# Performance work log

Measured on AMD Instinct MI355X. Metric: run time of the kernel, lower is better.

The kernel has to match this reference:

```python
import jax, jax.numpy as jnp
import numpy as np

NQ, N, C = 8192, 32768, 128


def setup_inputs() -> dict:
    key = jax.random.key(0)
    k1, k2, k3 = jax.random.split(key, 3)
    return {
        "query_pos": jax.random.normal(k1, (NQ, 3), dtype=jnp.float32),
        "neural_feat": jax.random.normal(k2, (N, C), dtype=jnp.float32),
        "neural_pos": jax.random.normal(k3, (N, 3), dtype=jnp.float32),
        "knn": 64,
    }


def _cdist(a, b):
    # Euclidean pairwise distances via the (|a|^2 + |b|^2 - 2ab) expansion.
    a2 = jnp.sum(a * a, axis=-1, keepdims=True)          # [N',1]
    b2 = jnp.sum(b * b, axis=-1)                          # [N]
    d2 = a2 + b2[None, :] - 2.0 * (a @ b.T)               # [N',N]
    return jnp.sqrt(jnp.maximum(d2, 1e-12))


def reference(query_pos, neural_feat, neural_pos, knn):
    dists = _cdist(query_pos, neural_pos)                 # [N',N]
    # torch.topk(largest=False, sorted=True) == top_k of negated dists.
    neg_vals, closest_ind = jax.lax.top_k(-dists, knn)    # [N',k]
    closest_dists = -neg_vals                             # ascending
    closest_feat = neural_feat[closest_ind]               # [N',k,C] gather
    inv_dist = 1.0 / (closest_dists + 1e-5)               # [N',k]
    retrieved_feat = jnp.sum(closest_feat * inv_dist[..., None], axis=1)  # [N',C]
    return retrieved_feat
```

## Files before the change

kernel.cpp:

```cpp
#include <hip/hip_runtime.h>
#include <math.h>

#define NQ    8192
#define NPTS  32768
#define KNN   64
#define CAP   256
#define PG    64
#define PNC   (PG*PG*PG)
#define PCELL 0.15f
#define PGINV (PG / 9.6f)
#define QG    32
#define QNC   (QG*QG*QG)
#define QGINV (QG / 9.6f)
#define GLO   (-4.8f)
#define NBLK  2048
#define TGT   (110.0f / 32768.0f)
#define PCHUNKS (PNC / 1024)
#define QCHUNKS (QNC / 1024)

__device__ __forceinline__ unsigned key_of(float f) {
  unsigned u = __float_as_uint(f);
  return (u & 0x80000000u) ? ~u : (u | 0x80000000u);
}
__device__ __forceinline__ float val_of(unsigned k) {
  unsigned u = (k & 0x80000000u) ? (k & 0x7fffffffu) : ~k;
  return __uint_as_float(u);
}
__device__ __forceinline__ int mbcnt64(unsigned long long m) {
  return __builtin_amdgcn_mbcnt_hi((unsigned)(m >> 32),
         __builtin_amdgcn_mbcnt_lo((unsigned)m, 0));
}
__device__ __forceinline__ float rflf(float x) {
  return __int_as_float(__builtin_amdgcn_readfirstlane(__float_as_int(x)));
}
__device__ __forceinline__ int rfli(int x) { return __builtin_amdgcn_readfirstlane(x); }

__device__ __forceinline__ float norm_cdf(float x) { return 0.5f * erfcf(-x * 0.70710678f); }
__device__ __forceinline__ float ball_mass(float mu, float r) {
  float a = r - mu, b = r + mu;
  float e = __expf(-0.5f * b * b) - __expf(-0.5f * a * a);
  return e / (mu * 2.50662827f) + norm_cdf(a) - norm_cdf(-mu) + norm_cdf(b) - norm_cdf(mu);
}

__device__ __forceinline__ int cidxP(float v) {
  int i = (int)floorf((v - GLO) * PGINV);
  return min(max(i, 0), PG - 1);
}
__device__ __forceinline__ int cidxQ(float v) {
  int i = (int)floorf((v - GLO) * QGINV);
  return min(max(i, 0), QG - 1);
}


__global__ __launch_bounds__(256) void hist_tau_kernel(
    const float* __restrict__ pos, const float* __restrict__ qpos,
    int* __restrict__ pcnt, int* __restrict__ qcnt, float* __restrict__ tau) {
  const int gid = blockIdx.x * 256 + threadIdx.x;
  const float x = pos[gid * 3 + 0], y = pos[gid * 3 + 1], z = pos[gid * 3 + 2];
  atomicAdd(&pcnt[(cidxP(z) * PG + cidxP(y)) * PG + cidxP(x)], 1);
  if (gid < NQ) {
    const float qx = qpos[gid * 3 + 0], qy = qpos[gid * 3 + 1], qz = qpos[gid * 3 + 2];
    atomicAdd(&qcnt[(cidxQ(qz) * QG + cidxQ(qy)) * QG + cidxQ(qx)], 1);
    const float b = qx * qx + qy * qy + qz * qz;
    const float mu = fmaxf(sqrtf(b), 0.05f);
    float lo = 0.f, hi = mu + 8.f;
    for (int i = 0; i < 16; ++i) {
      const float r = 0.5f * (lo + hi);
      if (ball_mass(mu, r) < TGT) lo = r; else hi = r;
    }
    tau[gid] = hi * hi;
  }
}

__global__ __launch_bounds__(256) void scanA(
    const int* __restrict__ pcnt, int* __restrict__ qcnt,
    int* __restrict__ cellStart, int* __restrict__ paux, int* __restrict__ qaux) {
  __shared__ int aux[256];
  const int t = threadIdx.x;
  const bool isP = (blockIdx.x < PCHUNKS);
  const int cb = isP ? blockIdx.x : (blockIdx.x - PCHUNKS);
  const int base = cb * 1024 + t * 4;
  const int4 q = isP ? ((const int4*)(pcnt + base))[0] : ((const int4*)(qcnt + base))[0];
  const int ts = q.x + q.y + q.z + q.w;
  aux[t] = ts;
  __syncthreads();
  for (int off = 1; off < 256; off <<= 1) {
    const int u = (t >= off) ? aux[t - off] : 0;
    __syncthreads();
    aux[t] += u;
    __syncthreads();
  }
  int run = t ? aux[t - 1] : 0;
  int4 w;
  w.x = run; run += q.x;
  w.y = run; run += q.y;
  w.z = run; run += q.z;
  w.w = run; run += q.w;
  if (isP) ((int4*)(cellStart + base))[0] = w;
  else     ((int4*)(qcnt + base))[0] = w;
  if (t == 255) { if (isP) paux[cb] = aux[255]; else qaux[cb] = aux[255]; }
}

__global__ __launch_bounds__(256) void scanC(
    int* __restrict__ pcnt, int* __restrict__ qcnt, int* __restrict__ cellStart,
    const int* __restrict__ paux, const int* __restrict__ qaux) {
  __shared__ int aux[256];
  const int t = threadIdx.x;
  const bool isP = (blockIdx.x < PCHUNKS);
  const int cb = isP ? blockIdx.x : (blockIdx.x - PCHUNKS);
  int v = 0;
  if (isP) { if (t < cb) v = paux[t]; }
  else     { if (t < cb && t < QCHUNKS) v = qaux[t]; }
  aux[t] = v;
  __syncthreads();
  for (int off = 128; off; off >>= 1) {
    if (t < off) aux[t] += aux[t + off];
    __syncthreads();
  }
  const int offc = aux[0];
  const int base = cb * 1024 + t * 4;
  if (isP) {
    int4 w = ((const int4*)(cellStart + base))[0];
    w.x += offc; w.y += offc; w.z += offc; w.w += offc;
    ((int4*)(cellStart + base))[0] = w;
    ((int4*)(pcnt + base))[0] = w;
    if (blockIdx.x == PCHUNKS - 1 && t == 255) cellStart[PNC] = NPTS;
  } else {
    int4 w = ((const int4*)(qcnt + base))[0];
    w.x += offc; w.y += offc; w.z += offc; w.w += offc;
    ((int4*)(qcnt + base))[0] = w;
  }
}

__global__ __launch_bounds__(256) void scatter_kernel(
    const float* __restrict__ pos, const float* __restrict__ qpos,
    int* __restrict__ pcur, int* __restrict__ qcur, const float* __restrict__ tau,
    float4* __restrict__ pts, float4* __restrict__ qp, float* __restrict__ qtau) {
  const int gid = blockIdx.x * 256 + threadIdx.x;
  const float x = pos[gid * 3 + 0], y = pos[gid * 3 + 1], z = pos[gid * 3 + 2];
  const int c = (cidxP(z) * PG + cidxP(y)) * PG + cidxP(x);
  const int slot = atomicAdd(&pcur[c], 1);
  pts[slot] = make_float4(x, y, z, __int_as_float(gid));
  if (gid < NQ) {
    const float a = qpos[gid * 3 + 0], b = qpos[gid * 3 + 1], d = qpos[gid * 3 + 2];
    const int qc = (cidxQ(d) * QG + cidxQ(b)) * QG + cidxQ(a);
    const int qs = atomicAdd(&qcur[qc], 1);
    qp[qs] = make_float4(a, b, d, __int_as_float(gid));
    qtau[qs] = tau[gid];
  }
}


__global__ __launch_bounds__(256, 8) void knn_main(
    const float* __restrict__ feat, const int* __restrict__ cellStart,
    const float4* __restrict__ pts, const float4* __restrict__ qp,
    const float* __restrict__ qtau, float* __restrict__ out) {

  __shared__ uint2 sCand[4][CAP];
  __shared__ uint2 sSel[4][KNN];

  const int tid = threadIdx.x, lane = tid & 63, wv = tid >> 6;
  const int bid = blockIdx.x;
  const int swz = (bid & 7) * (NBLK / 8) + (bid >> 3);
  const int sq  = swz * 4 + wv;

  const float4 Q = qp[sq];
  const float qx = rflf(Q.x), qy = rflf(Q.y), qz = rflf(Q.z);
  const int orig = rfli(__float_as_int(Q.w));
  const float bq = qx * qx + qy * qy + qz * qz;
  const float nx = -2.f * qx, ny = -2.f * qy, nz = -2.f * qz;
  float r2 = rflf(qtau[sq]);
  float tlo = 0.f, thi = -1.f;
  int cnt = 0;

  for (int attempt = 0; attempt < 12; ++attempt) {
    const float r = sqrtf(r2);
    const float tq = r2 - bq;
    const int iy0 = cidxP(qy - r), iy1 = cidxP(qy + r);
    const int iz0 = cidxP(qz - r), iz1 = cidxP(qz + r);
    const int nyw  = iy1 - iy0 + 1;
    const int nrow = nyw * (iz1 - iz0 + 1);
    cnt = 0;
    for (int rc = 0; rc < nrow; rc += 64) {
      const int myrow = rc + lane;
      int s = 0, c = 0;
      if (myrow < nrow) {
        const int dz = myrow / nyw;
        const int dy = myrow - dz * nyw;
        const int giy = iy0 + dy, giz = iz0 + dz;
        const float ylo = GLO + giy * PCELL;
        const float zlo = GLO + giz * PCELL;
        const float dyv = fmaxf(0.f, fmaxf(ylo - qy, qy - (ylo + PCELL)));
        const float dzv = fmaxf(0.f, fmaxf(zlo - qz, qz - (zlo + PCELL)));
        const float dd = dyv * dyv + dzv * dzv;
        if (dd < r2) {
          const float hx = sqrtf(r2 - dd);
          const int jx0 = cidxP(qx - hx), jx1 = cidxP(qx + hx);
          const int rb = (giz * PG + giy) * PG;
          s = cellStart[rb + jx0];
          c = cellStart[rb + jx1 + 1] - s;
        }
      }
      int cum = c;
      #pragma unroll
      for (int off = 1; off < 64; off <<= 1) {
        const int u = __shfl_up(cum, off);
        if (lane >= off) cum += u;
      }
      const int adj = s - (cum - c);
      const int Tc = __shfl(cum, 63);
      for (int b = 0; b < Tc; b += 64) {
        const int fi = b + lane;
        const bool have = fi < Tc;
        int ro = 0;
        #pragma unroll
        for (int st = 32; st; st >>= 1) {
          const int nr = ro + st;
          const int probe = __shfl(cum, min(nr, 64) - 1);
          if (nr <= 64 && probe <= fi) ro = nr;
        }
        const int pi = fi + __shfl(adj, min(ro, 63));
        const float4 P = pts[have ? pi : 0];
        const float n = P.x * P.x + P.y * P.y + P.z * P.z;
        const float d = fmaf(P.z, nz, fmaf(P.y, ny, fmaf(P.x, nx, n)));
        const bool hh = have && (d < tq);
        const unsigned long long m = __ballot(hh);
        if (m) {
          const int p = cnt + mbcnt64(m);
          if (hh && p < CAP)
            sCand[wv][p] = make_uint2(key_of(d + bq), __float_as_uint(P.w));
          cnt += (int)__popcll(m);
        }
      }
    }
    if (cnt >= KNN && cnt <= CAP) break;
    if (cnt < KNN) { tlo = r2; r2 = (thi < 0.f) ? r2 * 3.f : 0.5f * (r2 + thi); }
    else           { thi = r2; r2 = 0.5f * (tlo + r2); }
  }

  {
    const int mm = min(cnt, CAP);
    unsigned k[4], id[4];
    #pragma unroll
    for (int s = 0; s < 4; ++s) {
      const int g2 = s * 64 + lane;
      uint2 kv = make_uint2(0xFFFFFFFFu, 0u);
      if (g2 < mm) kv = sCand[wv][g2];
      k[s] = kv.x; id[s] = kv.y;
    }
    unsigned blo = 0x80000000u, bhi = 0xFFFFFFFFu;
    for (int it = 0; it < 32; ++it) {
      const unsigned mid = blo + ((bhi - blo) >> 1);
      const int c = (int)(__popcll(__ballot(k[0] <= mid)) + __popcll(__ballot(k[1] <= mid)) +
                          __popcll(__ballot(k[2] <= mid)) + __popcll(__ballot(k[3] <= mid)));
      if (c >= KNN) bhi = mid; else blo = mid + 1;
    }
    const unsigned K = blo;

    int fill = 0;
    #pragma unroll
    for (int s = 0; s < 4; ++s) {
      const bool lt = k[s] < K;
      const unsigned long long msk = __ballot(lt);
      if (msk) {
        const int p = fill + mbcnt64(msk);
        if (lt) { const float dv = val_of(k[s]);
                  const float w_ = 1.f / (sqrtf(fmaxf(dv, 1e-12f)) + 1e-5f);
                  sSel[wv][p] = make_uint2(id[s], __float_as_uint(w_)); }
        fill += (int)__popcll(msk);
      }
    }
    #pragma unroll
    for (int s = 0; s < 4; ++s) {
      const bool eq = (k[s] == K);
      const unsigned long long msk = __ballot(eq);
      if (msk) {
        const int p = fill + mbcnt64(msk);
        if (eq && p < KNN) { const float dv = val_of(k[s]);
                             const float w_ = 1.f / (sqrtf(fmaxf(dv, 1e-12f)) + 1e-5f);
                             sSel[wv][p] = make_uint2(id[s], __float_as_uint(w_)); }
        fill += (int)__popcll(msk);
      }
    }
  }

  {
    const int half = lane >> 5;
    const int col  = lane & 31;
    float4 acc = make_float4(0.f, 0.f, 0.f, 0.f);
    #pragma unroll 4
    for (int j = 0; j < KNN; j += 2) {
      const uint2 pr = sSel[wv][j + half];
      const float w = __uint_as_float(pr.y);
      const float4 f4 = *(const float4*)(feat + ((size_t)pr.x << 7) + (col << 2));
      acc.x = fmaf(w, f4.x, acc.x);
      acc.y = fmaf(w, f4.y, acc.y);
      acc.z = fmaf(w, f4.z, acc.z);
      acc.w = fmaf(w, f4.w, acc.w);
    }
    acc.x += __shfl_xor(acc.x, 32);
    acc.y += __shfl_xor(acc.y, 32);
    acc.z += __shfl_xor(acc.z, 32);
    acc.w += __shfl_xor(acc.w, 32);
    if (lane < 32)
      *(float4*)(out + ((size_t)orig << 7) + (col << 2)) = acc;
  }
}

extern "C" void kernel_launch(void* const* d_in, const int* in_sizes, int n_in,
                              void* d_out, int out_size, void* d_ws, size_t ws_size,
                              hipStream_t stream) {
  const float* qpos = (const float*)d_in[0];
  const float* feat = (const float*)d_in[1];
  const float* pos  = (const float*)d_in[2];
  float* out = (float*)d_out;

  char* ws = (char*)d_ws;
  int*    pcnt      = (int*)(ws);
  int*    qcnt      = (int*)(ws + (1024 << 10));
  int*    cellStart = (int*)(ws + (1152 << 10));
  float*  tau       = (float*)(ws + (2184 << 10));
  float4* pts       = (float4*)(ws + (2216 << 10));
  float4* qp        = (float4*)(ws + (2728 << 10));
  float*  qtau      = (float*)(ws + (2856 << 10));
  int*    paux      = (int*)(ws + (2888 << 10));
  int*    qaux      = (int*)(ws + (2889 << 10));

  hipMemsetAsync(ws, 0, 1152 << 10, stream);
  hist_tau_kernel<<<dim3(NPTS / 256),        dim3(256), 0, stream>>>(pos, qpos, pcnt, qcnt, tau);
  scanA          <<<dim3(PCHUNKS + QCHUNKS), dim3(256), 0, stream>>>(pcnt, qcnt, cellStart, paux, qaux);
  scanC          <<<dim3(PCHUNKS + QCHUNKS), dim3(256), 0, stream>>>(pcnt, qcnt, cellStart, paux, qaux);
  scatter_kernel <<<dim3(NPTS / 256),        dim3(256), 0, stream>>>(pos, qpos, pcnt, qcnt, tau, pts, qp, qtau);
  knn_main       <<<dim3(NBLK),              dim3(256), 0, stream>>>(feat, cellStart, pts, qp, qtau, out);
}
```

Measured before the change: 116.7 us.

## Fuse two-pass scan into single-pass scan with inter-block publish flags

Merges the two scan kernels into one. Each block publishes its chunk total (offset by one so zero means not ready) and spin-waits on the totals of earlier chunks to build its prefix offset. This removes one kernel launch and a global round trip over the count arrays. It relies on earlier blocks being resident or scheduled first to avoid deadlock (288 blocks, so likely fine on this GPU), and it widens the memset to clear the flag arrays.

```diff
diff --git a/kernel.cpp b/kernel.cpp
--- a/kernel.cpp
+++ b/kernel.cpp
@@ -72,62 +72,50 @@
   }
 }
 
-__global__ __launch_bounds__(256) void scanA(
-    const int* __restrict__ pcnt, int* __restrict__ qcnt,
-    int* __restrict__ cellStart, int* __restrict__ paux, int* __restrict__ qaux) {
+__global__ __launch_bounds__(256) void scan_kernel(
+    int* __restrict__ pcnt, int* __restrict__ qcnt, int* __restrict__ cellStart,
+    int* __restrict__ ppub, int* __restrict__ qpub) {
   __shared__ int aux[256];
+  __shared__ int off[256];
   const int t = threadIdx.x;
   const bool isP = (blockIdx.x < PCHUNKS);
   const int cb = isP ? blockIdx.x : (blockIdx.x - PCHUNKS);
+  int* src = isP ? pcnt : qcnt;
+  int* pub = isP ? ppub : qpub;
   const int base = cb * 1024 + t * 4;
-  const int4 q = isP ? ((const int4*)(pcnt + base))[0] : ((const int4*)(qcnt + base))[0];
-  const int ts = q.x + q.y + q.z + q.w;
-  aux[t] = ts;
+  const int4 q = ((const int4*)(src + base))[0];
+  aux[t] = q.x + q.y + q.z + q.w;
   __syncthreads();
-  for (int off = 1; off < 256; off <<= 1) {
-    const int u = (t >= off) ? aux[t - off] : 0;
+  for (int o = 1; o < 256; o <<= 1) {
+    const int u = (t >= o) ? aux[t - o] : 0;
     __syncthreads();
     aux[t] += u;
     __syncthreads();
   }
-  int run = t ? aux[t - 1] : 0;
+  if (t == 0) atomicExch(&pub[cb], aux[255] + 1);
+  int v = 0;
+  if (t < cb) {
+    while ((v = atomicOr(&pub[t], 0)) == 0) { }
+    v -= 1;
+  }
+  off[t] = v;
+  __syncthreads();
+  for (int o = 128; o; o >>= 1) {
+    if (t < o) off[t] += off[t + o];
+    __syncthreads();
+  }
+  const int chunkOff = off[0];
+  int run = (t ? aux[t - 1] : 0) + chunkOff;
   int4 w;
   w.x = run; run += q.x;
   w.y = run; run += q.y;
   w.z = run; run += q.z;
   w.w = run; run += q.w;
-  if (isP) ((int4*)(cellStart + base))[0] = w;
-  else     ((int4*)(qcnt + base))[0] = w;
-  if (t == 255) { if (isP) paux[cb] = aux[255]; else qaux[cb] = aux[255]; }
-}
-
-__global__ __launch_bounds__(256) void scanC(
-    int* __restrict__ pcnt, int* __restrict__ qcnt, int* __restrict__ cellStart,
-    const int* __restrict__ paux, const int* __restrict__ qaux) {
-  __shared__ int aux[256];
-  const int t = threadIdx.x;
-  const bool isP = (blockIdx.x < PCHUNKS);
-  const int cb = isP ? blockIdx.x : (blockIdx.x - PCHUNKS);
-  int v = 0;
-  if (isP) { if (t < cb) v = paux[t]; }
-  else     { if (t < cb && t < QCHUNKS) v = qaux[t]; }
-  aux[t] = v;
-  __syncthreads();
-  for (int off = 128; off; off >>= 1) {
-    if (t < off) aux[t] += aux[t + off];
-    __syncthreads();
-  }
-  const int offc = aux[0];
-  const int base = cb * 1024 + t * 4;
   if (isP) {
-    int4 w = ((const int4*)(cellStart + base))[0];
-    w.x += offc; w.y += offc; w.z += offc; w.w += offc;
     ((int4*)(cellStart + base))[0] = w;
     ((int4*)(pcnt + base))[0] = w;
-    if (blockIdx.x == PCHUNKS - 1 && t == 255) cellStart[PNC] = NPTS;
+    if (cb == PCHUNKS - 1 && t == 255) cellStart[PNC] = NPTS;
   } else {
-    int4 w = ((const int4*)(qcnt + base))[0];
-    w.x += offc; w.y += offc; w.z += offc; w.w += offc;
     ((int4*)(qcnt + base))[0] = w;
   }
 }
@@ -318,18 +306,17 @@
   char* ws = (char*)d_ws;
   int*    pcnt      = (int*)(ws);
   int*    qcnt      = (int*)(ws + (1024 << 10));
-  int*    cellStart = (int*)(ws + (1152 << 10));
-  float*  tau       = (float*)(ws + (2184 << 10));
-  float4* pts       = (float4*)(ws + (2216 << 10));
-  float4* qp        = (float4*)(ws + (2728 << 10));
-  float*  qtau      = (float*)(ws + (2856 << 10));
-  int*    paux      = (int*)(ws + (2888 << 10));
-  int*    qaux      = (int*)(ws + (2889 << 10));
-
-  hipMemsetAsync(ws, 0, 1152 << 10, stream);
+  int*    ppub      = (int*)(ws + (1152 << 10));
+  int*    qpub      = (int*)(ws + (1153 << 10));
+  int*    cellStart = (int*)(ws + (1156 << 10));
+  float*  tau       = (float*)(ws + (2188 << 10));
+  float4* pts       = (float4*)(ws + (2220 << 10));
+  float4* qp        = (float4*)(ws + (2732 << 10));
+  float*  qtau      = (float*)(ws + (2860 << 10));
+
+  hipMemsetAsync(ws, 0, 1154 << 10, stream);
   hist_tau_kernel<<<dim3(NPTS / 256),        dim3(256), 0, stream>>>(pos, qpos, pcnt, qcnt, tau);
-  scanA          <<<dim3(PCHUNKS + QCHUNKS), dim3(256), 0, stream>>>(pcnt, qcnt, cellStart, paux, qaux);
-  scanC          <<<dim3(PCHUNKS + QCHUNKS), dim3(256), 0, stream>>>(pcnt, qcnt, cellStart, paux, qaux);
+  scan_kernel    <<<dim3(PCHUNKS + QCHUNKS), dim3(256), 0, stream>>>(pcnt, qcnt, cellStart, ppub, qpub);
   scatter_kernel <<<dim3(NPTS / 256),        dim3(256), 0, stream>>>(pos, qpos, pcnt, qcnt, tau, pts, qp, qtau);
   knn_main       <<<dim3(NBLK),              dim3(256), 0, stream>>>(feat, cellStart, pts, qp, qtau, out);
 }
```

After: 118.4 us. About the same (+1.4%).
